# Optimization experiments

Measured on AMD Instinct MI355X. Metric: run time of the kernel, lower is better.

## Reference

```python
import jax, jax.numpy as jnp
import numpy as np

F_IN, N_TREES, DEPTH, TREE_DIM, BATCH = 256, 512, 6, 3, 512


def entmax15_axis0(z):
    """Exact 1.5-entmax along axis 0 (sort-based algorithm from Peters et al. 2019)."""
    z = z / 2.0
    z = z - jnp.max(z, axis=0, keepdims=True)
    zs = -jnp.sort(-z, axis=0)                      # descending sort, [F, N]
    F = z.shape[0]
    rho = jnp.arange(1, F + 1, dtype=z.dtype)[:, None]
    mean = jnp.cumsum(zs, axis=0) / rho
    mean_sq = jnp.cumsum(zs * zs, axis=0) / rho
    ss = rho * (mean_sq - mean * mean)
    delta = (1.0 - ss) / rho
    tau = mean - jnp.sqrt(jnp.clip(delta, 0.0))
    support = (tau <= zs).astype(jnp.int32)
    k = jnp.sum(support, axis=0) - 1                # last valid index per column
    tau_star = jnp.take_along_axis(tau, k[None, :], axis=0)
    return jnp.square(jnp.clip(z - tau_star, 0.0))


def setup_inputs() -> dict:
    key = jax.random.key(0)
    k0, k1, k2, k3 = jax.random.split(key, 4)
    return {
        "input": jax.random.normal(k0, (BATCH, F_IN), jnp.float32),
        "feat_attention": jax.random.uniform(k1, (F_IN, N_TREES * DEPTH), jnp.float32),
        "feature_thresholds": jax.random.normal(k2, (N_TREES, DEPTH), jnp.float32) * 0.1,
        "log_temperatures": jnp.zeros((N_TREES, DEPTH), jnp.float32),
        "response": jax.random.normal(k3, (N_TREES, TREE_DIM, 2 ** DEPTH), jnp.float32),
    }


def reference(input, feat_attention, feature_thresholds, log_temperatures, response):
    T, D = feature_thresholds.shape
    F = feat_attention.shape[0]
    # sparse feature selection per (tree, depth)
    choice_weight = entmax15_axis0(feat_attention).reshape(F, T, D)
    feature_values = jnp.einsum('bi,ind->bnd', input, choice_weight)      # [B, T, D]
    # thresholding with learned temperature, bin_func == '05_01'
    tl = (feature_values - feature_thresholds) * jnp.exp(-log_temperatures)
    tl = jnp.stack([-tl, tl], axis=-1)                                    # [B, T, D, 2]
    bins = jnp.clip(0.5 * tl + 0.5, -0.5, 1.5)
    # binary codes of the 2^D leaves: [D, 2^D, 2]
    idx = jnp.arange(2 ** D)
    off = 2 ** jnp.arange(D)
    bc = ((idx[None, :] // off[:, None]) % 2).astype(bins.dtype)
    codes = jnp.stack([bc, 1.0 - bc], axis=-1)
    # depth-wise outer product into leaf weights
    bin_matches = jnp.einsum('btds,dcs->btdc', bins, codes)               # [B, T, D, 2^D]
    response_weights = jnp.prod(bin_matches, axis=-2)                     # [B, T, 2^D]
    out = jnp.einsum('bnd,ncd->bnc', response_weights, response)          # [B, T, C]
    return out.reshape(out.shape[0], -1)
```

## Files before the change

### kernel.cpp

```cpp
#include <hip/hip_runtime.h>
#include <math.h>

#define F_IN 256
#define NTREES 512
#define DEPTH 6
#define NCOLS (NTREES * DEPTH)
#define BATCH 512
#define OUTW (NTREES * 3)

typedef __attribute__((ext_vector_type(8))) short bf16x8;
typedef __attribute__((ext_vector_type(4))) float f32x4;
typedef __attribute__((ext_vector_type(4))) unsigned short u16x4;
typedef __attribute__((ext_vector_type(8))) unsigned short u16x8;

__device__ __forceinline__ unsigned short f2bf(float x) {
    unsigned u = __float_as_uint(x);
    return (unsigned short)((u + 0x7FFFu + ((u >> 16) & 1u)) >> 16);
}
__device__ __forceinline__ void split2(float x, unsigned short& h, unsigned short& l) {
    h = f2bf(x);
    l = f2bf(x - __uint_as_float((unsigned)h << 16));
}

__global__ __launch_bounds__(256) void k_entmax(const float* __restrict__ att,
                                                const float* __restrict__ inp,
                                                unsigned short* __restrict__ cwT_hi,
                                                unsigned short* __restrict__ cwT_lo,
                                                unsigned short* __restrict__ in_hi,
                                                unsigned short* __restrict__ in_lo) {
    const int tid = threadIdx.x;

    if (blockIdx.x >= NCOLS / 16) {
        const int cb = blockIdx.x - NCOLS / 16;
        const float4* src = (const float4*)inp;
#pragma unroll
        for (int it = 0; it < 16; ++it) {
            int idx = cb * 4096 + it * 256 + tid;
            float4 v = src[idx];
            u16x4 h, l;
            unsigned short th, tl;
            split2(v.x, th, tl); h.x = th; l.x = tl;
            split2(v.y, th, tl); h.y = th; l.y = tl;
            split2(v.z, th, tl); h.z = th; l.z = tl;
            split2(v.w, th, tl); h.w = th; l.w = tl;
            *(u16x4*)&in_hi[idx * 4] = h;
            *(u16x4*)&in_lo[idx * 4] = l;
        }
        return;
    }

    const int n0 = blockIdx.x * 16;
    const int lane = tid & 63;
    const int w = tid >> 6;
    __shared__ float s_z[16][260];

    const int cld = tid & 15;
#pragma unroll
    for (int it = 0; it < 16; ++it) {
        int f = (tid >> 4) + it * 16;
        s_z[cld][f] = att[f * NCOLS + n0 + cld];
    }
    __syncthreads();

    float4 z[4];
    float m[4], tau[4];
#pragma unroll
    for (int c = 0; c < 4; ++c) {
        float4 v = *(const float4*)&s_z[w * 4 + c][4 * lane];
        z[c] = make_float4(v.x * 0.5f, v.y * 0.5f, v.z * 0.5f, v.w * 0.5f);
        m[c] = fmaxf(fmaxf(z[c].x, z[c].y), fmaxf(z[c].z, z[c].w));
    }
#pragma unroll
    for (int off = 32; off >= 1; off >>= 1)
#pragma unroll
        for (int c = 0; c < 4; ++c)
            m[c] = fmaxf(m[c], __shfl_xor(m[c], off));
#pragma unroll
    for (int c = 0; c < 4; ++c) {
        z[c].x -= m[c]; z[c].y -= m[c]; z[c].z -= m[c]; z[c].w -= m[c];
        tau[c] = -1.0f;
    }

    for (int iter = 0; iter < 14; ++iter) {
        float S1[4], S2[4];
#pragma unroll
        for (int c = 0; c < 4; ++c) {
            float d0 = fmaxf(z[c].x - tau[c], 0.f);
            float d1 = fmaxf(z[c].y - tau[c], 0.f);
            float d2 = fmaxf(z[c].z - tau[c], 0.f);
            float d3 = fmaxf(z[c].w - tau[c], 0.f);
            S1[c] = (d0 + d1) + (d2 + d3);
            S2[c] = fmaf(d0, d0, fmaf(d1, d1, fmaf(d2, d2, d3 * d3)));
        }
#pragma unroll
        for (int off = 32; off >= 1; off >>= 1)
#pragma unroll
            for (int c = 0; c < 4; ++c) {
                S1[c] += __shfl_xor(S1[c], off);
                S2[c] += __shfl_xor(S2[c], off);
            }
        bool done = true;
#pragma unroll
        for (int c = 0; c < 4; ++c) {
            tau[c] += (S2[c] - 1.f) / (2.f * S1[c]);
            done = done && (fabsf(S2[c] - 1.f) < 4e-6f);
        }
        if (done) break;
    }

#pragma unroll
    for (int c = 0; c < 4; ++c) {
        float4 pv;
        float v0 = fmaxf(z[c].x - tau[c], 0.f);
        float v1 = fmaxf(z[c].y - tau[c], 0.f);
        float v2 = fmaxf(z[c].z - tau[c], 0.f);
        float v3 = fmaxf(z[c].w - tau[c], 0.f);
        pv.x = v0 * v0; pv.y = v1 * v1; pv.z = v2 * v2; pv.w = v3 * v3;
        *(float4*)&s_z[w * 4 + c][4 * lane] = pv;
    }
    __syncthreads();
    const int nl = tid >> 4;
    const int f0 = (tid & 15) * 16;
#pragma unroll
    for (int j = 0; j < 2; ++j) {
        u16x8 hv, lv;
#pragma unroll
        for (int e = 0; e < 8; ++e) {
            unsigned short h, l;
            split2(s_z[nl][f0 + j * 8 + e], h, l);
            hv[e] = h; lv[e] = l;
        }
        *(u16x8*)&cwT_hi[(n0 + nl) * F_IN + f0 + j * 8] = hv;
        *(u16x8*)&cwT_lo[(n0 + nl) * F_IN + f0 + j * 8] = lv;
    }
}

__global__ __launch_bounds__(128) void k_gemm(const unsigned short* __restrict__ Ah,
                                              const unsigned short* __restrict__ Al,
                                              const unsigned short* __restrict__ Bh,
                                              const unsigned short* __restrict__ Bl,
                                              float* __restrict__ fv) {
    const int tid = threadIdx.x;
    const int wave = tid >> 6, lane = tid & 63;
    const int quad = lane >> 4, lr = lane & 15;
    const int n0 = blockIdx.x * 32;
    const int bw = blockIdx.y * 128 + wave * 64;

    const unsigned short* pah = Ah + (n0 + lr) * F_IN + quad * 8;
    const unsigned short* pal = Al + (n0 + lr) * F_IN + quad * 8;
    const unsigned short* pbh = Bh + (bw + lr) * F_IN + quad * 8;
    const unsigned short* pbl = Bl + (bw + lr) * F_IN + quad * 8;

    f32x4 acc[2][4];
#pragma unroll
    for (int i = 0; i < 2; ++i)
#pragma unroll
        for (int j = 0; j < 4; ++j)
            acc[i][j] = (f32x4){0.f, 0.f, 0.f, 0.f};

#pragma unroll
    for (int k0 = 0; k0 < F_IN; k0 += 32) {
        bf16x8 ah[2], al[2], bh[4], bl[4];
#pragma unroll
        for (int i = 0; i < 2; ++i) {
            ah[i] = *(const bf16x8*)(pah + i * 16 * F_IN + k0);
            al[i] = *(const bf16x8*)(pal + i * 16 * F_IN + k0);
        }
#pragma unroll
        for (int j = 0; j < 4; ++j) {
            bh[j] = *(const bf16x8*)(pbh + j * 16 * F_IN + k0);
            bl[j] = *(const bf16x8*)(pbl + j * 16 * F_IN + k0);
        }
#pragma unroll
        for (int i = 0; i < 2; ++i)
#pragma unroll
            for (int j = 0; j < 4; ++j) {
                acc[i][j] = __builtin_amdgcn_mfma_f32_16x16x32_bf16(ah[i], bh[j], acc[i][j], 0, 0, 0);
                acc[i][j] = __builtin_amdgcn_mfma_f32_16x16x32_bf16(ah[i], bl[j], acc[i][j], 0, 0, 0);
                acc[i][j] = __builtin_amdgcn_mfma_f32_16x16x32_bf16(al[i], bh[j], acc[i][j], 0, 0, 0);
            }
    }

#pragma unroll
    for (int i = 0; i < 2; ++i)
#pragma unroll
        for (int j = 0; j < 4; ++j)
#pragma unroll
            for (int r = 0; r < 4; ++r)
                fv[(n0 + 16 * i + quad * 4 + r) * BATCH + bw + 16 * j + lr] = acc[i][j][r];
}

__global__ __launch_bounds__(256) void k_tree(const float* __restrict__ fv,
                                              const float* __restrict__ thr,
                                              const float* __restrict__ ltemp,
                                              const float* __restrict__ resp,
                                              float* __restrict__ out) {
    const int t0 = blockIdx.x * 8;
    const int b0 = blockIdx.y * 64;
    const int tid = threadIdx.x;
    const int bl = tid & 63;
    const int b = b0 + bl;
    const int tsub = tid >> 6;
    __shared__ float s_resp[8 * 192];
    __shared__ float s_out[64][25];

    for (int i = tid; i < 8 * 192; i += 256)
        s_resp[i] = resp[t0 * 192 + i];
    __syncthreads();

#pragma unroll
    for (int half_t = 0; half_t < 2; ++half_t) {
        const int ttl = tsub + half_t * 4;
        const int tt = t0 + ttl;
        float bpos[6], bneg[6];
#pragma unroll
        for (int d = 0; d < 6; ++d) {
            float fvv = fv[(tt * 6 + d) * BATCH + b];
            float tl = (fvv - thr[tt * 6 + d]) * expf(-ltemp[tt * 6 + d]);
            float hp = 0.5f * tl + 0.5f;
            float hn = 0.5f - 0.5f * tl;
            bpos[d] = fminf(fmaxf(hp, -0.5f), 1.5f);
            bneg[d] = fminf(fmaxf(hn, -0.5f), 1.5f);
        }
        float p[64];
        p[0] = 1.f;
#pragma unroll
        for (int d = 0; d < 6; ++d) {
            int half = 1 << d;
#pragma unroll 32
            for (int i = half - 1; i >= 0; --i) {
                float v = p[i];
                p[i + half] = v * bneg[d];
                p[i]        = v * bpos[d];
            }
        }
        float a0 = 0.f, a1 = 0.f, a2 = 0.f;
        const float* r = &s_resp[ttl * 192];
#pragma unroll
        for (int c = 0; c < 64; ++c) {
            a0 = fmaf(p[c], r[c], a0);
            a1 = fmaf(p[c], r[64 + c], a1);
            a2 = fmaf(p[c], r[128 + c], a2);
        }
        s_out[bl][ttl * 3 + 0] = a0;
        s_out[bl][ttl * 3 + 1] = a1;
        s_out[bl][ttl * 3 + 2] = a2;
    }
    __syncthreads();
    for (int i = tid; i < 64 * 24; i += 256) {
        int row = i / 24, col = i % 24;
        out[(b0 + row) * OUTW + t0 * 3 + col] = s_out[row][col];
    }
}

extern "C" void kernel_launch(void* const* d_in, const int* in_sizes, int n_in,
                              void* d_out, int out_size, void* d_ws, size_t ws_size,
                              hipStream_t stream) {
    const float* input = (const float*)d_in[0];
    const float* att   = (const float*)d_in[1];
    const float* thr   = (const float*)d_in[2];
    const float* ltemp = (const float*)d_in[3];
    const float* resp  = (const float*)d_in[4];
    float* out = (float*)d_out;

    unsigned short* cwT_hi = (unsigned short*)d_ws;
    unsigned short* cwT_lo = cwT_hi + NCOLS * F_IN;
    unsigned short* in_hi  = cwT_lo + NCOLS * F_IN;
    unsigned short* in_lo  = in_hi + BATCH * F_IN;
    float* fv = (float*)(in_lo + BATCH * F_IN);

    hipLaunchKernelGGL(k_entmax, dim3(NCOLS / 16 + 8), dim3(256), 0, stream,
                       att, input, cwT_hi, cwT_lo, in_hi, in_lo);
    hipLaunchKernelGGL(k_gemm, dim3(NCOLS / 32, BATCH / 128), dim3(128), 0, stream,
                       cwT_hi, cwT_lo, in_hi, in_lo, fv);
    hipLaunchKernelGGL(k_tree, dim3(NTREES / 8, BATCH / 64), dim3(256), 0, stream,
                       fv, thr, ltemp, resp, out);
}
```

Measured before the change: 95.69 us.

## Fuse feature GEMM with tree evaluation through shared memory

Merges the split-bf16 MFMA GEMM and the tree leaf-weight kernel into one kernel. Each block computes feature values for 8 trees (48 columns) by 128 batch rows, stages them in LDS, and evaluates the trees directly. This removes the global round trip of the feature-value buffer and one kernel launch. In exchange the GEMM tiling changes (3x2 MFMA tiles per wave) and LDS use per block grows, which may lower occupancy; grid size drops to 256 blocks.

```diff
diff --git a/kernel.cpp b/kernel.cpp
--- a/kernel.cpp
+++ b/kernel.cpp
@@ -135,121 +135,120 @@
     }
 }
 
-__global__ __launch_bounds__(128) void k_gemm(const unsigned short* __restrict__ Ah,
-                                              const unsigned short* __restrict__ Al,
-                                              const unsigned short* __restrict__ Bh,
-                                              const unsigned short* __restrict__ Bl,
-                                              float* __restrict__ fv) {
+__global__ __launch_bounds__(256) void k_fused(const unsigned short* __restrict__ Ah,
+                                               const unsigned short* __restrict__ Al,
+                                               const unsigned short* __restrict__ Bh,
+                                               const unsigned short* __restrict__ Bl,
+                                               const float* __restrict__ thr,
+                                               const float* __restrict__ ltemp,
+                                               const float* __restrict__ resp,
+                                               float* __restrict__ out) {
+    const int tb  = blockIdx.x;
+    const int b0  = blockIdx.y * 128;
+    const int t0g = tb * 8;
+    const int n0g = tb * 48;
     const int tid = threadIdx.x;
     const int wave = tid >> 6, lane = tid & 63;
     const int quad = lane >> 4, lr = lane & 15;
-    const int n0 = blockIdx.x * 32;
-    const int bw = blockIdx.y * 128 + wave * 64;
-
-    const unsigned short* pah = Ah + (n0 + lr) * F_IN + quad * 8;
-    const unsigned short* pal = Al + (n0 + lr) * F_IN + quad * 8;
+
+    __shared__ float sFV[48][132];
+    __shared__ float sR[8 * 192];
+    __shared__ float sTH[48], sET[48];
+    __shared__ float sO[128][25];
+
+    for (int i = tid; i < 8 * 192; i += 256) sR[i] = resp[t0g * 192 + i];
+    if (tid < 48) {
+        sTH[tid] = thr[n0g + tid];
+        sET[tid] = expf(-ltemp[n0g + tid]);
+    }
+
+    const int bw = b0 + wave * 32;
+    const unsigned short* pah = Ah + (n0g + lr) * F_IN + quad * 8;
+    const unsigned short* pal = Al + (n0g + lr) * F_IN + quad * 8;
     const unsigned short* pbh = Bh + (bw + lr) * F_IN + quad * 8;
     const unsigned short* pbl = Bl + (bw + lr) * F_IN + quad * 8;
 
-    f32x4 acc[2][4];
-#pragma unroll
-    for (int i = 0; i < 2; ++i)
-#pragma unroll
-        for (int j = 0; j < 4; ++j)
+    f32x4 acc[3][2];
+#pragma unroll
+    for (int i = 0; i < 3; ++i)
+#pragma unroll
+        for (int j = 0; j < 2; ++j)
             acc[i][j] = (f32x4){0.f, 0.f, 0.f, 0.f};
 
 #pragma unroll
     for (int k0 = 0; k0 < F_IN; k0 += 32) {
-        bf16x8 ah[2], al[2], bh[4], bl[4];
-#pragma unroll
-        for (int i = 0; i < 2; ++i) {
+        bf16x8 ah[3], al[3], bh[2], bl[2];
+#pragma unroll
+        for (int i = 0; i < 3; ++i) {
             ah[i] = *(const bf16x8*)(pah + i * 16 * F_IN + k0);
             al[i] = *(const bf16x8*)(pal + i * 16 * F_IN + k0);
         }
 #pragma unroll
-        for (int j = 0; j < 4; ++j) {
+        for (int j = 0; j < 2; ++j) {
             bh[j] = *(const bf16x8*)(pbh + j * 16 * F_IN + k0);
             bl[j] = *(const bf16x8*)(pbl + j * 16 * F_IN + k0);
         }
 #pragma unroll
-        for (int i = 0; i < 2; ++i)
-#pragma unroll
-            for (int j = 0; j < 4; ++j) {
+        for (int i = 0; i < 3; ++i)
+#pragma unroll
+            for (int j = 0; j < 2; ++j) {
                 acc[i][j] = __builtin_amdgcn_mfma_f32_16x16x32_bf16(ah[i], bh[j], acc[i][j], 0, 0, 0);
                 acc[i][j] = __builtin_amdgcn_mfma_f32_16x16x32_bf16(ah[i], bl[j], acc[i][j], 0, 0, 0);
                 acc[i][j] = __builtin_amdgcn_mfma_f32_16x16x32_bf16(al[i], bh[j], acc[i][j], 0, 0, 0);
             }
     }
-
-#pragma unroll
-    for (int i = 0; i < 2; ++i)
-#pragma unroll
-        for (int j = 0; j < 4; ++j)
+#pragma unroll
+    for (int i = 0; i < 3; ++i)
+#pragma unroll
+        for (int j = 0; j < 2; ++j)
 #pragma unroll
             for (int r = 0; r < 4; ++r)
-                fv[(n0 + 16 * i + quad * 4 + r) * BATCH + bw + 16 * j + lr] = acc[i][j][r];
-}
-
-__global__ __launch_bounds__(256) void k_tree(const float* __restrict__ fv,
-                                              const float* __restrict__ thr,
-                                              const float* __restrict__ ltemp,
-                                              const float* __restrict__ resp,
-                                              float* __restrict__ out) {
-    const int t0 = blockIdx.x * 8;
-    const int b0 = blockIdx.y * 64;
-    const int tid = threadIdx.x;
-    const int bl = tid & 63;
-    const int b = b0 + bl;
-    const int tsub = tid >> 6;
-    __shared__ float s_resp[8 * 192];
-    __shared__ float s_out[64][25];
-
-    for (int i = tid; i < 8 * 192; i += 256)
-        s_resp[i] = resp[t0 * 192 + i];
-    __syncthreads();
-
-#pragma unroll
-    for (int half_t = 0; half_t < 2; ++half_t) {
-        const int ttl = tsub + half_t * 4;
-        const int tt = t0 + ttl;
+                sFV[16 * i + quad * 4 + r][wave * 32 + 16 * j + lr] = acc[i][j][r];
+    __syncthreads();
+
+#pragma unroll
+    for (int p = 0; p < 4; ++p) {
+        const int pi = p * 256 + tid;
+        const int tl = pi >> 7;
+        const int b  = pi & 127;
         float bpos[6], bneg[6];
 #pragma unroll
         for (int d = 0; d < 6; ++d) {
-            float fvv = fv[(tt * 6 + d) * BATCH + b];
-            float tl = (fvv - thr[tt * 6 + d]) * expf(-ltemp[tt * 6 + d]);
-            float hp = 0.5f * tl + 0.5f;
-            float hn = 0.5f - 0.5f * tl;
+            float fvv = sFV[tl * 6 + d][b];
+            float tlv = (fvv - sTH[tl * 6 + d]) * sET[tl * 6 + d];
+            float hp = 0.5f * tlv + 0.5f;
+            float hn = 0.5f - 0.5f * tlv;
             bpos[d] = fminf(fmaxf(hp, -0.5f), 1.5f);
             bneg[d] = fminf(fmaxf(hn, -0.5f), 1.5f);
         }
-        float p[64];
-        p[0] = 1.f;
+        float pr[64];
+        pr[0] = 1.f;
 #pragma unroll
         for (int d = 0; d < 6; ++d) {
             int half = 1 << d;
 #pragma unroll 32
             for (int i = half - 1; i >= 0; --i) {
-                float v = p[i];
-                p[i + half] = v * bneg[d];
-                p[i]        = v * bpos[d];
+                float v = pr[i];
+                pr[i + half] = v * bneg[d];
+                pr[i]        = v * bpos[d];
             }
         }
         float a0 = 0.f, a1 = 0.f, a2 = 0.f;
-        const float* r = &s_resp[ttl * 192];
+        const float* r = &sR[tl * 192];
 #pragma unroll
         for (int c = 0; c < 64; ++c) {
-            a0 = fmaf(p[c], r[c], a0);
-            a1 = fmaf(p[c], r[64 + c], a1);
-            a2 = fmaf(p[c], r[128 + c], a2);
-        }
-        s_out[bl][ttl * 3 + 0] = a0;
-        s_out[bl][ttl * 3 + 1] = a1;
-        s_out[bl][ttl * 3 + 2] = a2;
-    }
-    __syncthreads();
-    for (int i = tid; i < 64 * 24; i += 256) {
+            a0 = fmaf(pr[c], r[c], a0);
+            a1 = fmaf(pr[c], r[64 + c], a1);
+            a2 = fmaf(pr[c], r[128 + c], a2);
+        }
+        sO[b][tl * 3 + 0] = a0;
+        sO[b][tl * 3 + 1] = a1;
+        sO[b][tl * 3 + 2] = a2;
+    }
+    __syncthreads();
+    for (int i = tid; i < 128 * 24; i += 256) {
         int row = i / 24, col = i % 24;
-        out[(b0 + row) * OUTW + t0 * 3 + col] = s_out[row][col];
+        out[(b0 + row) * OUTW + t0g * 3 + col] = sO[row][col];
     }
 }
 
@@ -267,12 +266,9 @@
     unsigned short* cwT_lo = cwT_hi + NCOLS * F_IN;
     unsigned short* in_hi  = cwT_lo + NCOLS * F_IN;
     unsigned short* in_lo  = in_hi + BATCH * F_IN;
-    float* fv = (float*)(in_lo + BATCH * F_IN);
 
     hipLaunchKernelGGL(k_entmax, dim3(NCOLS / 16 + 8), dim3(256), 0, stream,
                        att, input, cwT_hi, cwT_lo, in_hi, in_lo);
-    hipLaunchKernelGGL(k_gemm, dim3(NCOLS / 32, BATCH / 128), dim3(128), 0, stream,
-                       cwT_hi, cwT_lo, in_hi, in_lo, fv);
-    hipLaunchKernelGGL(k_tree, dim3(NTREES / 8, BATCH / 64), dim3(256), 0, stream,
-                       fv, thr, ltemp, resp, out);
-}
+    hipLaunchKernelGGL(k_fused, dim3(NTREES / 8, BATCH / 128), dim3(256), 0, stream,
+                       cwT_hi, cwT_lo, in_hi, in_lo, thr, ltemp, resp, out);
+}
```

Result: faster. 91.39 us (-4.5%).
